# Performance work log

Measured on AMD Instinct MI355X. Metric: run time of the kernel, lower is better.

Reference implementation:

```python
import jax, jax.numpy as jnp
import numpy as np

D_FEAT, HID, N_LAYERS = 6, 64, 2
NEG_SLOPE = 0.01


def gru_layer(x_seq, W_ih, W_hh, b_ih, b_hh):
    # x_seq: [T, N, in]; PyTorch gate order r, z, n
    N = x_seq.shape[1]
    h0 = jnp.zeros((N, W_hh.shape[1]), x_seq.dtype)
    def step(h, x_t):
        gi = x_t @ W_ih.T + b_ih
        gh = h @ W_hh.T + b_hh
        i_r, i_z, i_n = jnp.split(gi, 3, axis=-1)
        h_r, h_z, h_n = jnp.split(gh, 3, axis=-1)
        r = jax.nn.sigmoid(i_r + h_r)
        z = jax.nn.sigmoid(i_z + h_z)
        n = jnp.tanh(i_n + r * h_n)
        h_new = (1.0 - z) * n + z * h
        return h_new, h_new
    _, ys = jax.lax.scan(step, h0, x_seq)
    return ys  # [T, N, H]


def setup_inputs() -> dict:
    key = jax.random.key(0)
    ks = jax.random.split(key, 16)
    N, T = 4000, 60
    x = jax.random.normal(ks[0], (N, D_FEAT * T), dtype=jnp.float32)
    relation_matrix = jax.random.randint(ks[1], (N, N, 8), 0, 2).astype(jnp.float32)
    s = 0.1
    p = {
        'W_ih0': jax.random.normal(ks[2], (3 * HID, D_FEAT), jnp.float32) * s,
        'W_hh0': jax.random.normal(ks[3], (3 * HID, HID), jnp.float32) * s,
        'b_ih0': jnp.zeros((3 * HID,), jnp.float32),
        'b_hh0': jnp.zeros((3 * HID,), jnp.float32),
        'W_ih1': jax.random.normal(ks[4], (3 * HID, HID), jnp.float32) * s,
        'W_hh1': jax.random.normal(ks[5], (3 * HID, HID), jnp.float32) * s,
        'b_ih1': jnp.zeros((3 * HID,), jnp.float32),
        'b_hh1': jnp.zeros((3 * HID,), jnp.float32),
        'W_0': jax.random.normal(ks[6], (2 * HID, 1), jnp.float32) * s,
        'b_0': jnp.zeros((), jnp.float32),
        'W_1': jax.random.normal(ks[7], (2 * HID, 1), jnp.float32) * s,
        'b_1': jnp.zeros((), jnp.float32),
        'W_2': jax.random.normal(ks[8], (2 * HID, 1), jnp.float32) * s,
        'b_2': jnp.zeros((), jnp.float32),
        'fc_w': jax.random.normal(ks[9], (1, 2 * HID), jnp.float32) * s,
        'fc_b': jnp.zeros((1,), jnp.float32),
    }
    return dict(x=x, relation_matrix=relation_matrix, **p)


def _head_softmax(h, W, b, mask):
    # weight[i,j] = leaky_relu(h_i @ W[:H] + h_j @ W[H:] + b); avoids [N,N,2H] concat
    H = h.shape[1]
    a = h @ W[:H]            # [N,1]
    c = h @ W[H:]            # [N,1]
    w = jax.nn.leaky_relu(a + c.T + b, NEG_SLOPE)  # [N,N]
    valid = jnp.where(mask == 0, -1000000.0, mask * w)
    return jax.nn.softmax(valid, axis=1)


def reference(x, relation_matrix, W_ih0, W_hh0, b_ih0, b_hh0, W_ih1, W_hh1, b_ih1, b_hh1,
              W_0, b_0, W_1, b_1, W_2, b_2, fc_w, fc_b):
    N = x.shape[0]
    xs = x.reshape(N, D_FEAT, -1).transpose(2, 0, 1)  # [T, N, d_feat]
    y1 = gru_layer(xs, W_ih0, W_hh0, b_ih0, b_hh0)
    y2 = gru_layer(y1, W_ih1, W_hh1, b_ih1, b_hh1)
    h = y2[-1]  # [N, H] last time step
    mask = jnp.sum(relation_matrix, axis=2)  # [N, N]
    s0 = _head_softmax(h, W_0, b_0, mask)
    s1 = _head_softmax(h, W_1, b_1, mask)
    s2 = _head_softmax(h, W_2, b_2, mask)
    agg = ((s0 + s1 + s2) / 3.0) @ h  # [N, H]
    hid = jnp.concatenate([h, agg], axis=1)  # [N, 2H]
    pred = (hid @ fc_w.T + fc_b).squeeze(-1)  # [N]
    return pred
```

## Files before the change

### kernel.cpp

```cpp
#include <hip/hip_runtime.h>

typedef __attribute__((ext_vector_type(8))) short bf16x8;
typedef __attribute__((ext_vector_type(4))) float f32x4;
typedef __attribute__((ext_vector_type(4))) float f4v;

__device__ __forceinline__ unsigned short f2bf(float f){
  unsigned u = __builtin_bit_cast(unsigned, f);
  u += 0x7FFFu + ((u >> 16) & 1u);
  return (unsigned short)(u >> 16);
}
__device__ __forceinline__ float bf2f(unsigned short b){
  unsigned u = ((unsigned)b) << 16;
  return __builtin_bit_cast(float, u);
}
__device__ __forceinline__ float sigmoidf_(float x){ return 1.f/(1.f + __expf(-x)); }
__device__ __forceinline__ float tanhf_(float x){
  float a = fabsf(x);
  float t = __expf(-2.f*a);
  float r = (1.f - t)/(1.f + t);
  return copysignf(r, x);
}

struct WF { bf16x8 hi, lo; };

__device__ __forceinline__ f32x4 mm3(bf16x8 ah, bf16x8 al, const WF& B, f32x4 D){
  D = __builtin_amdgcn_mfma_f32_16x16x32_bf16(al, B.hi, D, 0, 0, 0);
  D = __builtin_amdgcn_mfma_f32_16x16x32_bf16(ah, B.lo, D, 0, 0, 0);
  D = __builtin_amdgcn_mfma_f32_16x16x32_bf16(ah, B.hi, D, 0, 0, 0);
  return D;
}

__device__ __forceinline__ WF load_wf(const float* W, int ldk, int row, int k0, int kmax){
  WF f;
  #pragma unroll
  for (int j = 0; j < 8; j++){
    int k = k0 + j;
    float v = (k < kmax) ? W[row*ldk + k] : 0.f;
    unsigned short hb = f2bf(v);
    f.hi[j] = (short)hb;
    f.lo[j] = (short)f2bf(v - bf2f(hb));
  }
  return f;
}

__global__ __launch_bounds__(256, 1)
void gru_kernel(const float* __restrict__ x,
                const float* __restrict__ Wih0, const float* __restrict__ Whh0,
                const float* __restrict__ bih0, const float* __restrict__ bhh0,
                const float* __restrict__ Wih1, const float* __restrict__ Whh1,
                const float* __restrict__ bih1, const float* __restrict__ bhh1,
                float* __restrict__ hfin){
  __shared__ unsigned short xp_hi[16][60][8];
  __shared__ unsigned short xp_lo[16][60][8];
  __shared__ unsigned short h0hi[16][72], h0lo[16][72], h1hi[16][72], h1lo[16][72];

  const int tid  = threadIdx.x;
  const int lane = tid & 63;
  const int w    = tid >> 6;
  const int c    = lane & 15;
  const int q    = lane >> 4;
  const int d    = w*16 + c;
  const int nbase = blockIdx.x * 16;

  for (int v = tid; v < 16*360; v += 256){
    int n = v / 360, rem = v % 360;
    int dd = rem / 60, tt = rem % 60;
    float f = x[(size_t)(nbase + n)*360 + rem];
    unsigned short hb = f2bf(f);
    xp_hi[n][tt][dd] = hb;
    xp_lo[n][tt][dd] = f2bf(f - bf2f(hb));
  }
  for (int v = tid; v < 16*60*2; v += 256){
    int n = v / 120, rem = v % 120;
    int tt = rem >> 1, dd = 6 + (rem & 1);
    xp_hi[n][tt][dd] = 0; xp_lo[n][tt][dd] = 0;
  }
  for (int v = tid; v < 16*72; v += 256){
    int n = v / 72, k = v % 72;
    h0hi[n][k] = 0; h0lo[n][k] = 0; h1hi[n][k] = 0; h1lo[n][k] = 0;
  }

  const float bi0r = bih0[d], bi0z = bih0[64+d], bi0n = bih0[128+d];
  const float bh0r = bhh0[d], bh0z = bhh0[64+d], bh0n = bhh0[128+d];
  const float bi1r = bih1[d], bi1z = bih1[64+d], bi1n = bih1[128+d];
  const float bh1r = bhh1[d], bh1z = bhh1[64+d], bh1n = bhh1[128+d];

  WF Bih0[3];
  WF Bhh0[3][2], Bih1[3][2], Bhh1[3][2];
  #pragma unroll
  for (int g = 0; g < 3; g++){
    int row = g*64 + d;
    Bih0[g] = load_wf(Wih0, 6, row, q*8, 6);
    #pragma unroll
    for (int kt = 0; kt < 2; kt++){
      Bhh0[g][kt] = load_wf(Whh0, 64, row, kt*32 + q*8, 64);
      Bih1[g][kt] = load_wf(Wih1, 64, row, kt*32 + q*8, 64);
      Bhh1[g][kt] = load_wf(Whh1, 64, row, kt*32 + q*8, 64);
    }
  }

  float h0old[4] = {0,0,0,0}, h1old[4] = {0,0,0,0};

  __syncthreads();

  #pragma unroll 1
  for (int t = 0; t < 60; t++){
    bf16x8 a_h0h[2], a_h0l[2], a_h1h[2], a_h1l[2];
    #pragma unroll
    for (int kt = 0; kt < 2; kt++){
      a_h0h[kt] = *(const bf16x8*)&h0hi[c][kt*32 + q*8];
      a_h0l[kt] = *(const bf16x8*)&h0lo[c][kt*32 + q*8];
      a_h1h[kt] = *(const bf16x8*)&h1hi[c][kt*32 + q*8];
      a_h1l[kt] = *(const bf16x8*)&h1lo[c][kt*32 + q*8];
    }
    bf16x8 a_xh = {}, a_xl = {};
    if (q == 0){
      a_xh = *(const bf16x8*)&xp_hi[c][t][0];
      a_xl = *(const bf16x8*)&xp_lo[c][t][0];
    }
    __syncthreads();

    f32x4 Dr = {0,0,0,0}, Dz = {0,0,0,0}, Dni = {0,0,0,0}, Dnh = {0,0,0,0};
    Dr  = mm3(a_xh, a_xl, Bih0[0], Dr);
    Dz  = mm3(a_xh, a_xl, Bih0[1], Dz);
    Dni = mm3(a_xh, a_xl, Bih0[2], Dni);
    #pragma unroll
    for (int kt = 0; kt < 2; kt++){
      Dr  = mm3(a_h0h[kt], a_h0l[kt], Bhh0[0][kt], Dr);
      Dz  = mm3(a_h0h[kt], a_h0l[kt], Bhh0[1][kt], Dz);
      Dnh = mm3(a_h0h[kt], a_h0l[kt], Bhh0[2][kt], Dnh);
    }
    #pragma unroll
    for (int rI = 0; rI < 4; rI++){
      float rv = sigmoidf_(Dr[rI] + bi0r + bh0r);
      float zv = sigmoidf_(Dz[rI] + bi0z + bh0z);
      float nv = tanhf_(Dni[rI] + bi0n + rv*(Dnh[rI] + bh0n));
      float hnew = (1.f - zv)*nv + zv*h0old[rI];
      h0old[rI] = hnew;
      unsigned short hb = f2bf(hnew);
      int node = q*4 + rI;
      h0hi[node][d] = hb;
      h0lo[node][d] = f2bf(hnew - bf2f(hb));
    }
    __syncthreads();

    bf16x8 a_yh[2], a_yl[2];
    #pragma unroll
    for (int kt = 0; kt < 2; kt++){
      a_yh[kt] = *(const bf16x8*)&h0hi[c][kt*32 + q*8];
      a_yl[kt] = *(const bf16x8*)&h0lo[c][kt*32 + q*8];
    }
    f32x4 Er = {0,0,0,0}, Ez = {0,0,0,0}, Eni = {0,0,0,0}, Enh = {0,0,0,0};
    #pragma unroll
    for (int kt = 0; kt < 2; kt++){
      Er  = mm3(a_yh[kt], a_yl[kt], Bih1[0][kt], Er);
      Ez  = mm3(a_yh[kt], a_yl[kt], Bih1[1][kt], Ez);
      Eni = mm3(a_yh[kt], a_yl[kt], Bih1[2][kt], Eni);
      Er  = mm3(a_h1h[kt], a_h1l[kt], Bhh1[0][kt], Er);
      Ez  = mm3(a_h1h[kt], a_h1l[kt], Bhh1[1][kt], Ez);
      Enh = mm3(a_h1h[kt], a_h1l[kt], Bhh1[2][kt], Enh);
    }
    #pragma unroll
    for (int rI = 0; rI < 4; rI++){
      float rv = sigmoidf_(Er[rI] + bi1r + bh1r);
      float zv = sigmoidf_(Ez[rI] + bi1z + bh1z);
      float nv = tanhf_(Eni[rI] + bi1n + rv*(Enh[rI] + bh1n));
      float hnew = (1.f - zv)*nv + zv*h1old[rI];
      h1old[rI] = hnew;
      unsigned short hb = f2bf(hnew);
      int node = q*4 + rI;
      h1hi[node][d] = hb;
      h1lo[node][d] = f2bf(hnew - bf2f(hb));
    }
    __syncthreads();
  }

  #pragma unroll
  for (int rI = 0; rI < 4; rI++){
    int node = nbase + q*4 + rI;
    hfin[(size_t)node*64 + d] = h1old[rI];
  }
}

__global__ void ac_kernel(const float* __restrict__ hfin,
                          const float* __restrict__ W0h, const float* __restrict__ W1h,
                          const float* __restrict__ W2h, float* __restrict__ ac){
  int lane = threadIdx.x & 63;
  int node = blockIdx.x*4 + (threadIdx.x >> 6);
  float hv = hfin[(size_t)node*64 + lane];
  const float* Ws[3] = {W0h, W1h, W2h};
  #pragma unroll
  for (int h = 0; h < 3; h++){
    float pa = hv * Ws[h][lane];
    float pc = hv * Ws[h][64 + lane];
    #pragma unroll
    for (int m = 32; m >= 1; m >>= 1){
      pa += __shfl_xor(pa, m, 64);
      pc += __shfl_xor(pc, m, 64);
    }
    if (lane == 0){
      ac[(size_t)(2*h)*4000 + node]   = pa;
      ac[(size_t)(2*h+1)*4000 + node] = pc;
    }
  }
}

__global__ __launch_bounds__(256, 4)
void attn2_kernel(const float* __restrict__ rel, const float* __restrict__ hfin,
                  const float* __restrict__ ac,
                  const float* __restrict__ b0p, const float* __restrict__ b1p,
                  const float* __restrict__ b2p,
                  const float* __restrict__ fcw, const float* __restrict__ fcb,
                  float* __restrict__ pred){
  __shared__ float m0[4000], m1[4000];
  __shared__ float red[4][8];
  __shared__ float aggred[4][2][64];

  const int tid  = threadIdx.x;
  const int lane = tid & 63;
  const int w    = tid >> 6;
  const int i0   = blockIdx.x * 2;
  const float b0 = b0p[0], b1 = b1p[0], b2 = b2p[0];
  const float bh[3] = {b0, b1, b2};

  const float* c0 = ac + 1*4000;
  const float* c1 = ac + 3*4000;
  const float* c2 = ac + 5*4000;

  float ai[2][3];
  #pragma unroll
  for (int r = 0; r < 2; r++)
    #pragma unroll
    for (int h = 0; h < 3; h++)
      ai[r][h] = ac[(size_t)(2*h)*4000 + i0 + r];

  float z[2][3] = {{0.f,0.f,0.f},{0.f,0.f,0.f}};

  for (int j = tid; j < 4000; j += 256){
    const f4v* rp0 = (const f4v*)(rel + ((size_t)i0*4000 + j)*8);
    const f4v* rp1 = (const f4v*)(rel + ((size_t)(i0+1)*4000 + j)*8);
    f4v a0 = __builtin_nontemporal_load(rp0);
    f4v a1 = __builtin_nontemporal_load(rp0 + 1);
    f4v a2 = __builtin_nontemporal_load(rp1);
    f4v a3 = __builtin_nontemporal_load(rp1 + 1);
    float mk0 = a0[0]+a0[1]+a0[2]+a0[3] + a1[0]+a1[1]+a1[2]+a1[3];
    float mk1 = a2[0]+a2[1]+a2[2]+a2[3] + a3[0]+a3[1]+a3[2]+a3[3];
    m0[j] = mk0; m1[j] = mk1;
    float cv[3] = {c0[j], c1[j], c2[j]};
    #pragma unroll
    for (int h = 0; h < 3; h++){
      float s0 = ai[0][h] + cv[h] + bh[h];
      float s1 = ai[1][h] + cv[h] + bh[h];
      float w0 = s0 > 0.f ? s0 : 0.01f*s0;
      float w1 = s1 > 0.f ? s1 : 0.01f*s1;
      float v0 = (mk0 == 0.f) ? -1e6f : mk0*w0;
      float v1 = (mk1 == 0.f) ? -1e6f : mk1*w1;
      z[0][h] += __expf(v0);
      z[1][h] += __expf(v1);
    }
  }
  #pragma unroll
  for (int r = 0; r < 2; r++)
    #pragma unroll
    for (int h = 0; h < 3; h++){
      float v = z[r][h];
      #pragma unroll
      for (int m = 32; m >= 1; m >>= 1) v += __shfl_xor(v, m, 64);
      if (lane == 0) red[w][r*3 + h] = v;
    }
  __syncthreads();
  float iZ[2][3];
  #pragma unroll
  for (int r = 0; r < 2; r++)
    #pragma unroll
    for (int h = 0; h < 3; h++)
      iZ[r][h] = 1.f/(red[0][r*3+h] + red[1][r*3+h] + red[2][r*3+h] + red[3][r*3+h]);

  for (int j = tid; j < 4000; j += 256){
    float mk0 = m0[j], mk1 = m1[j];
    float cv[3] = {c0[j], c1[j], c2[j]};
    float w0s = 0.f, w1s = 0.f;
    #pragma unroll
    for (int h = 0; h < 3; h++){
      float s0 = ai[0][h] + cv[h] + bh[h];
      float s1 = ai[1][h] + cv[h] + bh[h];
      float w0 = s0 > 0.f ? s0 : 0.01f*s0;
      float w1 = s1 > 0.f ? s1 : 0.01f*s1;
      float v0 = (mk0 == 0.f) ? -1e6f : mk0*w0;
      float v1 = (mk1 == 0.f) ? -1e6f : mk1*w1;
      w0s += __expf(v0) * iZ[0][h];
      w1s += __expf(v1) * iZ[1][h];
    }
    m0[j] = w0s * (1.f/3.f);
    m1[j] = w1s * (1.f/3.f);
  }
  __syncthreads();

  float acc0 = 0.f, acc1 = 0.f;
  const int jb = w * 1000;
  #pragma unroll 4
  for (int jj = 0; jj < 1000; jj++){
    int j = jb + jj;
    float hv = hfin[(size_t)j*64 + lane];
    acc0 = fmaf(m0[j], hv, acc0);
    acc1 = fmaf(m1[j], hv, acc1);
  }
  aggred[w][0][lane] = acc0;
  aggred[w][1][lane] = acc1;
  __syncthreads();
  if (tid < 128){
    int r = tid >> 6, d = tid & 63;
    float agg = aggred[0][r][d] + aggred[1][r][d] + aggred[2][r][d] + aggred[3][r][d];
    float term = hfin[(size_t)(i0+r)*64 + d]*fcw[d] + agg*fcw[64 + d];
    #pragma unroll
    for (int m = 32; m >= 1; m >>= 1) term += __shfl_xor(term, m, 64);
    if (d == 0) pred[i0 + r] = term + fcb[0];
  }
}

extern "C" void kernel_launch(void* const* d_in, const int* in_sizes, int n_in,
                              void* d_out, int out_size, void* d_ws, size_t ws_size,
                              hipStream_t stream) {
  const float* x    = (const float*)d_in[0];
  const float* rel  = (const float*)d_in[1];
  const float* Wih0 = (const float*)d_in[2];
  const float* Whh0 = (const float*)d_in[3];
  const float* bih0 = (const float*)d_in[4];
  const float* bhh0 = (const float*)d_in[5];
  const float* Wih1 = (const float*)d_in[6];
  const float* Whh1 = (const float*)d_in[7];
  const float* bih1 = (const float*)d_in[8];
  const float* bhh1 = (const float*)d_in[9];
  const float* W0   = (const float*)d_in[10];
  const float* b0   = (const float*)d_in[11];
  const float* W1   = (const float*)d_in[12];
  const float* b1   = (const float*)d_in[13];
  const float* W2   = (const float*)d_in[14];
  const float* b2   = (const float*)d_in[15];
  const float* fcw  = (const float*)d_in[16];
  const float* fcb  = (const float*)d_in[17];
  float* pred = (float*)d_out;
  float* hfin = (float*)d_ws;
  float* ac   = hfin + 4000*64;

  gru_kernel<<<dim3(250), dim3(256), 0, stream>>>(x, Wih0, Whh0, bih0, bhh0,
                                                  Wih1, Whh1, bih1, bhh1, hfin);
  ac_kernel<<<dim3(1000), dim3(256), 0, stream>>>(hfin, W0, W1, W2, ac);
  attn2_kernel<<<dim3(2000), dim3(256), 0, stream>>>(rel, hfin, ac, b0, b1, b2,
                                                     fcw, fcb, pred);
}
```

Measured before the change: 907.0 us.

## Double-buffer GRU hidden state, split MFMA chains, prefetch relation rows

The GRU kernel keeps two copies of the layer-0 and layer-1 hidden state in shared memory, ping-ponged by timestep parity. This removes two of the three barriers per step. Each split-bf16 matmul now accumulates into separate hi and lo accumulators, which shortens dependent MFMA chains but doubles the accumulator registers. The attention kernel software-prefetches the next relation rows, reads softmax weights as float4, reuses m0 for the cross-wave reduction, and lowers the occupancy hint from 4 to 3.

```diff
diff --git a/kernel.cpp b/kernel.cpp
--- a/kernel.cpp
+++ b/kernel.cpp
@@ -23,11 +23,11 @@
 
 struct WF { bf16x8 hi, lo; };
 
-__device__ __forceinline__ f32x4 mm3(bf16x8 ah, bf16x8 al, const WF& B, f32x4 D){
-  D = __builtin_amdgcn_mfma_f32_16x16x32_bf16(al, B.hi, D, 0, 0, 0);
-  D = __builtin_amdgcn_mfma_f32_16x16x32_bf16(ah, B.lo, D, 0, 0, 0);
-  D = __builtin_amdgcn_mfma_f32_16x16x32_bf16(ah, B.hi, D, 0, 0, 0);
-  return D;
+__device__ __forceinline__ void mmsplit(bf16x8 ah, bf16x8 al, const WF& B,
+                                        f32x4& Dh, f32x4& Dl){
+  Dh = __builtin_amdgcn_mfma_f32_16x16x32_bf16(ah, B.hi, Dh, 0, 0, 0);
+  Dl = __builtin_amdgcn_mfma_f32_16x16x32_bf16(al, B.hi, Dl, 0, 0, 0);
+  Dl = __builtin_amdgcn_mfma_f32_16x16x32_bf16(ah, B.lo, Dl, 0, 0, 0);
 }
 
 __device__ __forceinline__ WF load_wf(const float* W, int ldk, int row, int k0, int kmax){
@@ -52,7 +52,8 @@
                 float* __restrict__ hfin){
   __shared__ unsigned short xp_hi[16][60][8];
   __shared__ unsigned short xp_lo[16][60][8];
-  __shared__ unsigned short h0hi[16][72], h0lo[16][72], h1hi[16][72], h1lo[16][72];
+  __shared__ unsigned short h0hi[2][16][72], h0lo[2][16][72];
+  __shared__ unsigned short h1hi[2][16][72], h1lo[2][16][72];
 
   const int tid  = threadIdx.x;
   const int lane = tid & 63;
@@ -75,9 +76,9 @@
     int tt = rem >> 1, dd = 6 + (rem & 1);
     xp_hi[n][tt][dd] = 0; xp_lo[n][tt][dd] = 0;
   }
-  for (int v = tid; v < 16*72; v += 256){
-    int n = v / 72, k = v % 72;
-    h0hi[n][k] = 0; h0lo[n][k] = 0; h1hi[n][k] = 0; h1lo[n][k] = 0;
+  for (int v = tid; v < 2*16*72; v += 256){
+    ((unsigned short*)h0hi)[v] = 0; ((unsigned short*)h0lo)[v] = 0;
+    ((unsigned short*)h1hi)[v] = 0; ((unsigned short*)h1lo)[v] = 0;
   }
 
   const float bi0r = bih0[d], bi0z = bih0[64+d], bi0n = bih0[128+d];
@@ -105,74 +106,81 @@
 
   #pragma unroll 1
   for (int t = 0; t < 60; t++){
-    bf16x8 a_h0h[2], a_h0l[2], a_h1h[2], a_h1l[2];
-    #pragma unroll
-    for (int kt = 0; kt < 2; kt++){
-      a_h0h[kt] = *(const bf16x8*)&h0hi[c][kt*32 + q*8];
-      a_h0l[kt] = *(const bf16x8*)&h0lo[c][kt*32 + q*8];
-      a_h1h[kt] = *(const bf16x8*)&h1hi[c][kt*32 + q*8];
-      a_h1l[kt] = *(const bf16x8*)&h1lo[c][kt*32 + q*8];
+    const int p  = t & 1;
+    const int qb = p ^ 1;
+
+    bf16x8 a_h0h[2], a_h0l[2];
+    #pragma unroll
+    for (int kt = 0; kt < 2; kt++){
+      a_h0h[kt] = *(const bf16x8*)&h0hi[p][c][kt*32 + q*8];
+      a_h0l[kt] = *(const bf16x8*)&h0lo[p][c][kt*32 + q*8];
     }
     bf16x8 a_xh = {}, a_xl = {};
     if (q == 0){
       a_xh = *(const bf16x8*)&xp_hi[c][t][0];
       a_xl = *(const bf16x8*)&xp_lo[c][t][0];
     }
-    __syncthreads();
-
-    f32x4 Dr = {0,0,0,0}, Dz = {0,0,0,0}, Dni = {0,0,0,0}, Dnh = {0,0,0,0};
-    Dr  = mm3(a_xh, a_xl, Bih0[0], Dr);
-    Dz  = mm3(a_xh, a_xl, Bih0[1], Dz);
-    Dni = mm3(a_xh, a_xl, Bih0[2], Dni);
-    #pragma unroll
-    for (int kt = 0; kt < 2; kt++){
-      Dr  = mm3(a_h0h[kt], a_h0l[kt], Bhh0[0][kt], Dr);
-      Dz  = mm3(a_h0h[kt], a_h0l[kt], Bhh0[1][kt], Dz);
-      Dnh = mm3(a_h0h[kt], a_h0l[kt], Bhh0[2][kt], Dnh);
+
+    f32x4 RH = {0,0,0,0}, RL = {0,0,0,0};
+    f32x4 ZH = {0,0,0,0}, ZL = {0,0,0,0};
+    f32x4 NIH = {0,0,0,0}, NIL = {0,0,0,0};
+    f32x4 NHH = {0,0,0,0}, NHL = {0,0,0,0};
+    mmsplit(a_xh, a_xl, Bih0[0], RH, RL);
+    mmsplit(a_xh, a_xl, Bih0[1], ZH, ZL);
+    mmsplit(a_xh, a_xl, Bih0[2], NIH, NIL);
+    #pragma unroll
+    for (int kt = 0; kt < 2; kt++){
+      mmsplit(a_h0h[kt], a_h0l[kt], Bhh0[0][kt], RH, RL);
+      mmsplit(a_h0h[kt], a_h0l[kt], Bhh0[1][kt], ZH, ZL);
+      mmsplit(a_h0h[kt], a_h0l[kt], Bhh0[2][kt], NHH, NHL);
     }
     #pragma unroll
     for (int rI = 0; rI < 4; rI++){
-      float rv = sigmoidf_(Dr[rI] + bi0r + bh0r);
-      float zv = sigmoidf_(Dz[rI] + bi0z + bh0z);
-      float nv = tanhf_(Dni[rI] + bi0n + rv*(Dnh[rI] + bh0n));
+      float rv = sigmoidf_(RH[rI] + RL[rI] + bi0r + bh0r);
+      float zv = sigmoidf_(ZH[rI] + ZL[rI] + bi0z + bh0z);
+      float nv = tanhf_(NIH[rI] + NIL[rI] + bi0n + rv*(NHH[rI] + NHL[rI] + bh0n));
       float hnew = (1.f - zv)*nv + zv*h0old[rI];
       h0old[rI] = hnew;
       unsigned short hb = f2bf(hnew);
       int node = q*4 + rI;
-      h0hi[node][d] = hb;
-      h0lo[node][d] = f2bf(hnew - bf2f(hb));
+      h0hi[qb][node][d] = hb;
+      h0lo[qb][node][d] = f2bf(hnew - bf2f(hb));
     }
     __syncthreads();
 
-    bf16x8 a_yh[2], a_yl[2];
-    #pragma unroll
-    for (int kt = 0; kt < 2; kt++){
-      a_yh[kt] = *(const bf16x8*)&h0hi[c][kt*32 + q*8];
-      a_yl[kt] = *(const bf16x8*)&h0lo[c][kt*32 + q*8];
-    }
-    f32x4 Er = {0,0,0,0}, Ez = {0,0,0,0}, Eni = {0,0,0,0}, Enh = {0,0,0,0};
-    #pragma unroll
-    for (int kt = 0; kt < 2; kt++){
-      Er  = mm3(a_yh[kt], a_yl[kt], Bih1[0][kt], Er);
-      Ez  = mm3(a_yh[kt], a_yl[kt], Bih1[1][kt], Ez);
-      Eni = mm3(a_yh[kt], a_yl[kt], Bih1[2][kt], Eni);
-      Er  = mm3(a_h1h[kt], a_h1l[kt], Bhh1[0][kt], Er);
-      Ez  = mm3(a_h1h[kt], a_h1l[kt], Bhh1[1][kt], Ez);
-      Enh = mm3(a_h1h[kt], a_h1l[kt], Bhh1[2][kt], Enh);
+    bf16x8 a_yh[2], a_yl[2], a_h1h[2], a_h1l[2];
+    #pragma unroll
+    for (int kt = 0; kt < 2; kt++){
+      a_yh[kt]  = *(const bf16x8*)&h0hi[qb][c][kt*32 + q*8];
+      a_yl[kt]  = *(const bf16x8*)&h0lo[qb][c][kt*32 + q*8];
+      a_h1h[kt] = *(const bf16x8*)&h1hi[p][c][kt*32 + q*8];
+      a_h1l[kt] = *(const bf16x8*)&h1lo[p][c][kt*32 + q*8];
+    }
+    f32x4 EH = {0,0,0,0}, EL = {0,0,0,0};
+    f32x4 FH = {0,0,0,0}, FL = {0,0,0,0};
+    f32x4 GIH = {0,0,0,0}, GIL = {0,0,0,0};
+    f32x4 GHH = {0,0,0,0}, GHL = {0,0,0,0};
+    #pragma unroll
+    for (int kt = 0; kt < 2; kt++){
+      mmsplit(a_yh[kt], a_yl[kt], Bih1[0][kt], EH, EL);
+      mmsplit(a_yh[kt], a_yl[kt], Bih1[1][kt], FH, FL);
+      mmsplit(a_yh[kt], a_yl[kt], Bih1[2][kt], GIH, GIL);
+      mmsplit(a_h1h[kt], a_h1l[kt], Bhh1[0][kt], EH, EL);
+      mmsplit(a_h1h[kt], a_h1l[kt], Bhh1[1][kt], FH, FL);
+      mmsplit(a_h1h[kt], a_h1l[kt], Bhh1[2][kt], GHH, GHL);
     }
     #pragma unroll
     for (int rI = 0; rI < 4; rI++){
-      float rv = sigmoidf_(Er[rI] + bi1r + bh1r);
-      float zv = sigmoidf_(Ez[rI] + bi1z + bh1z);
-      float nv = tanhf_(Eni[rI] + bi1n + rv*(Enh[rI] + bh1n));
+      float rv = sigmoidf_(EH[rI] + EL[rI] + bi1r + bh1r);
+      float zv = sigmoidf_(FH[rI] + FL[rI] + bi1z + bh1z);
+      float nv = tanhf_(GIH[rI] + GIL[rI] + bi1n + rv*(GHH[rI] + GHL[rI] + bh1n));
       float hnew = (1.f - zv)*nv + zv*h1old[rI];
       h1old[rI] = hnew;
       unsigned short hb = f2bf(hnew);
       int node = q*4 + rI;
-      h1hi[node][d] = hb;
-      h1lo[node][d] = f2bf(hnew - bf2f(hb));
-    }
-    __syncthreads();
+      h1hi[qb][node][d] = hb;
+      h1lo[qb][node][d] = f2bf(hnew - bf2f(hb));
+    }
   }
 
   #pragma unroll
@@ -205,7 +213,7 @@
   }
 }
 
-__global__ __launch_bounds__(256, 4)
+__global__ __launch_bounds__(256, 3)
 void attn2_kernel(const float* __restrict__ rel, const float* __restrict__ hfin,
                   const float* __restrict__ ac,
                   const float* __restrict__ b0p, const float* __restrict__ b1p,
@@ -214,14 +222,12 @@
                   float* __restrict__ pred){
   __shared__ float m0[4000], m1[4000];
   __shared__ float red[4][8];
-  __shared__ float aggred[4][2][64];
 
   const int tid  = threadIdx.x;
   const int lane = tid & 63;
   const int w    = tid >> 6;
   const int i0   = blockIdx.x * 2;
-  const float b0 = b0p[0], b1 = b1p[0], b2 = b2p[0];
-  const float bh[3] = {b0, b1, b2};
+  const float bh[3] = {b0p[0], b1p[0], b2p[0]};
 
   const float* c0 = ac + 1*4000;
   const float* c1 = ac + 3*4000;
@@ -236,27 +242,47 @@
 
   float z[2][3] = {{0.f,0.f,0.f},{0.f,0.f,0.f}};
 
-  for (int j = tid; j < 4000; j += 256){
-    const f4v* rp0 = (const f4v*)(rel + ((size_t)i0*4000 + j)*8);
-    const f4v* rp1 = (const f4v*)(rel + ((size_t)(i0+1)*4000 + j)*8);
-    f4v a0 = __builtin_nontemporal_load(rp0);
-    f4v a1 = __builtin_nontemporal_load(rp0 + 1);
-    f4v a2 = __builtin_nontemporal_load(rp1);
-    f4v a3 = __builtin_nontemporal_load(rp1 + 1);
-    float mk0 = a0[0]+a0[1]+a0[2]+a0[3] + a1[0]+a1[1]+a1[2]+a1[3];
-    float mk1 = a2[0]+a2[1]+a2[2]+a2[3] + a3[0]+a3[1]+a3[2]+a3[3];
-    m0[j] = mk0; m1[j] = mk1;
-    float cv[3] = {c0[j], c1[j], c2[j]};
-    #pragma unroll
-    for (int h = 0; h < 3; h++){
-      float s0 = ai[0][h] + cv[h] + bh[h];
-      float s1 = ai[1][h] + cv[h] + bh[h];
-      float w0 = s0 > 0.f ? s0 : 0.01f*s0;
-      float w1 = s1 > 0.f ? s1 : 0.01f*s1;
-      float v0 = (mk0 == 0.f) ? -1e6f : mk0*w0;
-      float v1 = (mk1 == 0.f) ? -1e6f : mk1*w1;
-      z[0][h] += __expf(v0);
-      z[1][h] += __expf(v1);
+  {
+    int j = tid;
+    bool have = (j < 4000);
+    f4v r0, r1, r2, r3;
+    if (have){
+      const f4v* rp0 = (const f4v*)(rel + ((size_t)i0*4000 + j)*8);
+      const f4v* rp1 = (const f4v*)(rel + ((size_t)(i0+1)*4000 + j)*8);
+      r0 = __builtin_nontemporal_load(rp0);
+      r1 = __builtin_nontemporal_load(rp0 + 1);
+      r2 = __builtin_nontemporal_load(rp1);
+      r3 = __builtin_nontemporal_load(rp1 + 1);
+    }
+    while (have){
+      int jn = j + 256;
+      bool haven = (jn < 4000);
+      f4v n0, n1, n2, n3;
+      if (haven){
+        const f4v* rp0 = (const f4v*)(rel + ((size_t)i0*4000 + jn)*8);
+        const f4v* rp1 = (const f4v*)(rel + ((size_t)(i0+1)*4000 + jn)*8);
+        n0 = __builtin_nontemporal_load(rp0);
+        n1 = __builtin_nontemporal_load(rp0 + 1);
+        n2 = __builtin_nontemporal_load(rp1);
+        n3 = __builtin_nontemporal_load(rp1 + 1);
+      }
+      float mk0 = r0[0]+r0[1]+r0[2]+r0[3] + r1[0]+r1[1]+r1[2]+r1[3];
+      float mk1 = r2[0]+r2[1]+r2[2]+r2[3] + r3[0]+r3[1]+r3[2]+r3[3];
+      m0[j] = mk0; m1[j] = mk1;
+      float cv[3] = {c0[j], c1[j], c2[j]};
+      #pragma unroll
+      for (int h = 0; h < 3; h++){
+        float s0 = ai[0][h] + cv[h] + bh[h];
+        float s1 = ai[1][h] + cv[h] + bh[h];
+        float w0 = s0 > 0.f ? s0 : 0.01f*s0;
+        float w1 = s1 > 0.f ? s1 : 0.01f*s1;
+        float v0 = (mk0 == 0.f) ? -1e6f : mk0*w0;
+        float v1 = (mk1 == 0.f) ? -1e6f : mk1*w1;
+        z[0][h] += __expf(v0);
+        z[1][h] += __expf(v1);
+      }
+      r0 = n0; r1 = n1; r2 = n2; r3 = n3;
+      j = jn; have = haven;
     }
   }
   #pragma unroll
@@ -298,19 +324,26 @@
 
   float acc0 = 0.f, acc1 = 0.f;
   const int jb = w * 1000;
-  #pragma unroll 4
-  for (int jj = 0; jj < 1000; jj++){
-    int j = jb + jj;
-    float hv = hfin[(size_t)j*64 + lane];
-    acc0 = fmaf(m0[j], hv, acc0);
-    acc1 = fmaf(m1[j], hv, acc1);
-  }
-  aggred[w][0][lane] = acc0;
-  aggred[w][1][lane] = acc1;
+  for (int jj = 0; jj < 1000; jj += 4){
+    float4 w0 = *(const float4*)&m0[jb + jj];
+    float4 w1 = *(const float4*)&m1[jb + jj];
+    float w0a[4] = {w0.x, w0.y, w0.z, w0.w};
+    float w1a[4] = {w1.x, w1.y, w1.z, w1.w};
+    #pragma unroll
+    for (int k = 0; k < 4; k++){
+      float hv = hfin[(size_t)(jb + jj + k)*64 + lane];
+      acc0 = fmaf(w0a[k], hv, acc0);
+      acc1 = fmaf(w1a[k], hv, acc1);
+    }
+  }
+  __syncthreads();
+  m0[(w*2 + 0)*64 + lane] = acc0;
+  m0[(w*2 + 1)*64 + lane] = acc1;
   __syncthreads();
   if (tid < 128){
     int r = tid >> 6, d = tid & 63;
-    float agg = aggred[0][r][d] + aggred[1][r][d] + aggred[2][r][d] + aggred[3][r][d];
+    float agg = m0[(0*2+r)*64 + d] + m0[(1*2+r)*64 + d]
+              + m0[(2*2+r)*64 + d] + m0[(3*2+r)*64 + d];
     float term = hfin[(size_t)(i0+r)*64 + d]*fcw[d] + agg*fcw[64 + d];
     #pragma unroll
     for (int m = 32; m >= 1; m >>= 1) term += __shfl_xor(term, m, 64);
```

After: 882.2 us. 2.7% less time.
